# Optimization experiments

Hardware: AMD Instinct MI355X
Metric: run time of the kernel (lower is better)

## Reference

```python
import jax, jax.numpy as jnp
import numpy as np

B, C, H, W = 8192, 3, 32, 32
IN_FEATURES = C * H * W  # 3072, hardcoded in the module


def setup_inputs() -> dict:
    key = jax.random.key(0)
    k1, k2 = jax.random.split(key)
    x = jax.random.normal(k1, (B, C, H, W), dtype=jnp.float32)
    noise = jax.random.normal(k2, (B, C, H, W), dtype=jnp.float32)  # randn_like(x)
    logvar_t = jnp.array([-1.0], dtype=jnp.float32)  # nn.Parameter init
    return {"x": x, "noise": noise, "logvar_t": logvar_t}


def reference(x, noise, logvar_t):
    # additive branch of view_learner.forward
    n_batch = x.shape[0]
    x_t = x + jnp.exp(0.5 * logvar_t[0]) * noise
    var = jnp.exp(logvar_t[0]) + 1e-10
    xf = x.reshape(n_batch, IN_FEATURES)
    # compute_distances: x_norm + x_t_norm - 2 * x @ x.T, clamped to [0, inf)
    x_norm = jnp.sum(xf * xf, axis=1)  # [B]
    dist = x_norm[:, None] + x_norm[None, :] - 2.0 * (xf @ xf.T)  # [B, B]
    dist = jnp.maximum(dist, 0.0)
    distance_contribution = -jnp.mean(jax.nn.logsumexp(-0.5 * dist / var, axis=1))
    normalization_constant = jnp.log(jnp.float32(n_batch))
    kl_xt = (normalization_constant + distance_contribution) / jnp.log(jnp.float32(2.0))
    return x_t, kl_xt
```

## Files before the change

kernel.cpp:

```cpp
#include <hip/hip_runtime.h>
#include <cstdint>

#define K_DIM 3072
#define B_DIM 8192
#define ROW_B 3072
#define ROW_U 768
#define BT    128
#define NTT   64
#define NKT   48

typedef __attribute__((ext_vector_type(4))) float f32x4;
typedef __attribute__((ext_vector_type(4))) int   i32x4;

#define QS     16.0f
#define INV_S2 0.00390625f

__device__ __forceinline__ int q8(float f) {
    int q = __float2int_rn(f * QS);
    return max(-127, min(127, q));
}
__device__ __forceinline__ unsigned pack4(float a, float b, float c, float d) {
    return (unsigned)(q8(a) & 0xFF)
         | ((unsigned)(q8(b) & 0xFF) << 8)
         | ((unsigned)(q8(c) & 0xFF) << 16)
         | ((unsigned)(q8(d) & 0xFF) << 24);
}

__global__ __launch_bounds__(384) void prep_kernel(const float* __restrict__ x,
                                                   const float* __restrict__ nz,
                                                   const float* __restrict__ logvar,
                                                   float* __restrict__ xt,
                                                   unsigned int* __restrict__ xb,
                                                   float* __restrict__ xn,
                                                   float* __restrict__ se)
{
    const int row = blockIdx.x;
    const int tid = threadIdx.x;
    const float4* xr = (const float4*)(x + (size_t)row * K_DIM);
    float4 v0 = xr[2 * tid];
    float4 v1 = xr[2 * tid + 1];
    float s = v0.x * v0.x + v0.y * v0.y + v0.z * v0.z + v0.w * v0.w
            + v1.x * v1.x + v1.y * v1.y + v1.z * v1.z + v1.w * v1.w;

    if (xt) {
        const float4* nr = (const float4*)(nz + (size_t)row * K_DIM);
        float4 n0 = nr[2 * tid], n1 = nr[2 * tid + 1];
        const float sc = __expf(0.5f * logvar[0]);
        float4 o0, o1;
        o0.x = fmaf(sc, n0.x, v0.x); o0.y = fmaf(sc, n0.y, v0.y);
        o0.z = fmaf(sc, n0.z, v0.z); o0.w = fmaf(sc, n0.w, v0.w);
        o1.x = fmaf(sc, n1.x, v1.x); o1.y = fmaf(sc, n1.y, v1.y);
        o1.z = fmaf(sc, n1.z, v1.z); o1.w = fmaf(sc, n1.w, v1.w);
        float4* tr = (float4*)(xt + (size_t)row * K_DIM);
        tr[2 * tid] = o0;
        tr[2 * tid + 1] = o1;
    }

    unsigned int* dst = xb + (size_t)row * ROW_U + tid * 2;
    dst[0] = pack4(v0.x, v0.y, v0.z, v0.w);
    dst[1] = pack4(v1.x, v1.y, v1.z, v1.w);

#pragma unroll
    for (int d = 32; d > 0; d >>= 1) s += __shfl_down(s, d);
    __shared__ float red[6];
    if ((tid & 63) == 0) red[tid >> 6] = s;
    __syncthreads();
    if (tid == 0) {
        float t = 0.f;
#pragma unroll
        for (int i = 0; i < 6; ++i) t += red[i];
        xn[row] = t;
        se[row] = 0.f;
    }
}

struct Frags { i32x4 a[4]; i32x4 b[4]; };

__global__ __launch_bounds__(256, 3) void gram_lse_kernel(const unsigned int* __restrict__ xb,
                                                          const float* __restrict__ xn,
                                                          const float* __restrict__ logvar,
                                                          float* __restrict__ se)
{
    __shared__ __align__(1024) unsigned char lds[3][16384];

    int rem = blockIdx.x;
    int bm = 0;
    while (rem >= NTT - bm) { rem -= NTT - bm; ++bm; }
    const int bn = bm + rem;

    const int tid  = threadIdx.x;
    const int lane = tid & 63;
    const int wave = tid >> 6;
    const int wr = wave >> 1, wc = wave & 1;
    const int fc = lane >> 4;

    const size_t rowA0 = (size_t)bm * BT;
    const size_t rowB0 = (size_t)bn * BT;
    const unsigned char* xb8 = (const unsigned char*)xb;

    unsigned int srcOff[4];
    int dstOff[4];
#pragma unroll
    for (int l = 0; l < 4; ++l) {
        const int e = (l & 1) * 256 + tid;
        const int r = e >> 2, c = e & 3;
        const int csw = c ^ ((r >> 1) & 3);
        const size_t rb = ((l < 2) ? rowA0 : rowB0) + (size_t)r;
        srcOff[l] = (unsigned int)(rb * ROW_B + (size_t)csw * 16);
        dstOff[l] = ((l < 2) ? 0 : 8192) + e * 16;
    }

    i32x4 acc[4][4];
#pragma unroll
    for (int i = 0; i < 4; ++i)
#pragma unroll
        for (int j = 0; j < 4; ++j) acc[i][j] = (i32x4){0, 0, 0, 0};

    int aOff[4], bOff[4];
#pragma unroll
    for (int mi = 0; mi < 4; ++mi) {
        const int r = wr * 64 + mi * 16 + (lane & 15);
        aOff[mi] = r * 64 + (fc ^ ((r >> 1) & 3)) * 16;
    }
#pragma unroll
    for (int ni = 0; ni < 4; ++ni) {
        const int r = wc * 64 + ni * 16 + (lane & 15);
        bOff[ni] = 8192 + r * 64 + (fc ^ ((r >> 1) & 3)) * 16;
    }

#pragma unroll
    for (int l = 0; l < 4; ++l)
        __builtin_amdgcn_global_load_lds(
            (const __attribute__((address_space(1))) void*)(xb8 + srcOff[l]),
            (__attribute__((address_space(3))) void*)(&lds[0][0] + dstOff[l]), 16, 0, 0);
#pragma unroll
    for (int l = 0; l < 4; ++l)
        __builtin_amdgcn_global_load_lds(
            (const __attribute__((address_space(1))) void*)(xb8 + srcOff[l] + 64u),
            (__attribute__((address_space(3))) void*)(&lds[1][0] + dstOff[l]), 16, 0, 0);
    asm volatile("s_waitcnt vmcnt(4)" ::: "memory");
    asm volatile("s_barrier" ::: "memory");

    Frags fA, fB;
#pragma unroll
    for (int mi = 0; mi < 4; ++mi) fA.a[mi] = *(const i32x4*)(&lds[0][0] + aOff[mi]);
#pragma unroll
    for (int ni = 0; ni < 4; ++ni) fA.b[ni] = *(const i32x4*)(&lds[0][0] + bOff[ni]);

    auto body = [&](int t, Frags& cur, Frags& nxt) {
        if (t + 2 < NKT) {
            unsigned char* buf = &lds[(t + 2) % 3][0];
            const unsigned int kg = (unsigned int)(t + 2) * 64u;
#pragma unroll
            for (int l = 0; l < 4; ++l)
                __builtin_amdgcn_global_load_lds(
                    (const __attribute__((address_space(1))) void*)(xb8 + srcOff[l] + kg),
                    (__attribute__((address_space(3))) void*)(buf + dstOff[l]), 16, 0, 0);
        }
        asm volatile("s_waitcnt lgkmcnt(0)" ::: "memory");
        if (t + 2 < NKT)
            asm volatile("s_waitcnt vmcnt(4)" ::: "memory");
        else
            asm volatile("s_waitcnt vmcnt(0)" ::: "memory");
        asm volatile("s_barrier" ::: "memory");
        if (t + 1 < NKT) {
            const unsigned char* buf = &lds[(t + 1) % 3][0];
#pragma unroll
            for (int mi = 0; mi < 4; ++mi) nxt.a[mi] = *(const i32x4*)(buf + aOff[mi]);
#pragma unroll
            for (int ni = 0; ni < 4; ++ni) nxt.b[ni] = *(const i32x4*)(buf + bOff[ni]);
        }
        __builtin_amdgcn_s_setprio(1);
#pragma unroll
        for (int mi = 0; mi < 4; ++mi)
#pragma unroll
            for (int ni = 0; ni < 4; ++ni)
                acc[mi][ni] = __builtin_amdgcn_mfma_i32_16x16x64_i8(
                    cur.a[mi], cur.b[ni], acc[mi][ni], 0, 0, 0);
        __builtin_amdgcn_s_setprio(0);
    };

    for (int tt = 0; tt < NKT / 2; ++tt) {
        body(2 * tt,     fA, fB);
        body(2 * tt + 1, fB, fA);
    }

    const float lv  = logvar[0];
    const float var = __expf(lv) + 1e-10f;
    const float cc  = 0.5f / var;

    const int colBase = (int)rowB0 + wc * 64 + (lane & 15);
    const int rowBase = (int)rowA0 + wr * 64 + (lane >> 4) * 4;

#pragma unroll
    for (int mi = 0; mi < 4; ++mi) {
#pragma unroll
        for (int rg = 0; rg < 4; ++rg) {
            const int i = rowBase + mi * 16 + rg;
            const float xni = xn[i];
            float rs = 0.f;
#pragma unroll
            for (int ni = 0; ni < 4; ++ni) {
                const int j = colBase + ni * 16;
                const float g = (float)acc[mi][ni][rg] * INV_S2;
                const float dist = xni + xn[j] - 2.f * g;
                rs += (i == j) ? 1.0f : __expf(-cc * fmaxf(dist, 0.f));
            }
#pragma unroll
            for (int d = 1; d < 16; d <<= 1) rs += __shfl_xor(rs, d);
            if ((lane & 15) == 0) atomicAdd(&se[i], rs);
        }
    }

    if (bm != bn) {
#pragma unroll
        for (int ni = 0; ni < 4; ++ni) {
            const int j = colBase + ni * 16;
            const float xnj = xn[j];
            float cs = 0.f;
#pragma unroll
            for (int mi = 0; mi < 4; ++mi)
#pragma unroll
                for (int rg = 0; rg < 4; ++rg) {
                    const int i = rowBase + mi * 16 + rg;
                    const float g = (float)acc[mi][ni][rg] * INV_S2;
                    cs += __expf(-cc * fmaxf(xn[i] + xnj - 2.f * g, 0.f));
                }
#pragma unroll
            for (int d = 16; d < 64; d <<= 1) cs += __shfl_xor(cs, d);
            if ((lane >> 4) == 0) atomicAdd(&se[j], cs);
        }
    }
}

__global__ __launch_bounds__(256) void kl_kernel(const float* __restrict__ se,
                                                 float* __restrict__ out)
{
    const int tid = threadIdx.x;
    float s = 0.f;
    for (int i = tid; i < B_DIM; i += 256) s += logf(se[i]);
#pragma unroll
    for (int d = 32; d > 0; d >>= 1) s += __shfl_down(s, d);
    __shared__ float red[4];
    if ((tid & 63) == 0) red[tid >> 6] = s;
    __syncthreads();
    if (tid == 0) {
        const float dc = -(red[0] + red[1] + red[2] + red[3]) / (float)B_DIM;
        out[0] = (logf((float)B_DIM) + dc) / logf(2.f);
    }
}

__global__ __launch_bounds__(256) void xt_kernel(const float4* __restrict__ x,
                                                 const float4* __restrict__ nz,
                                                 const float* __restrict__ logvar,
                                                 float4* __restrict__ out, int n4)
{
    const float sc = expf(0.5f * logvar[0]);
    for (int i = blockIdx.x * blockDim.x + threadIdx.x; i < n4;
         i += gridDim.x * blockDim.x) {
        float4 va = x[i], vb = nz[i];
        float4 o;
        o.x = fmaf(sc, vb.x, va.x);
        o.y = fmaf(sc, vb.y, va.y);
        o.z = fmaf(sc, vb.z, va.z);
        o.w = fmaf(sc, vb.w, va.w);
        out[i] = o;
    }
}

extern "C" void kernel_launch(void* const* d_in, const int* in_sizes, int n_in,
                              void* d_out, int out_size, void* d_ws, size_t ws_size,
                              hipStream_t stream)
{
    const float* x      = (const float*)d_in[0];
    const float* noise  = (const float*)d_in[1];
    const float* logvar = (const float*)d_in[2];
    float* out = (float*)d_out;

    const size_t NEL      = (size_t)B_DIM * K_DIM;
    const size_t XB_BYTES = (size_t)B_DIM * ROW_B;
    const int    NTILES   = NTT * (NTT + 1) / 2;

    const bool use_ws = ws_size >= XB_BYTES + 2 * (size_t)B_DIM * sizeof(float) + 256;

    if (use_ws) {
        unsigned int* xb = (unsigned int*)d_ws;
        float* xn = (float*)((char*)d_ws + XB_BYTES);
        float* se = xn + B_DIM;

        prep_kernel<<<B_DIM, 384, 0, stream>>>(x, noise, logvar, out, xb, xn, se);
        gram_lse_kernel<<<NTILES, 256, 0, stream>>>(xb, xn, logvar, se);
        kl_kernel<<<1, 256, 0, stream>>>(se, out + NEL);
    } else {
        unsigned int* xb = (unsigned int*)d_out;
        float* xn = (float*)((char*)d_out + (32u << 20));
        float* se = xn + B_DIM;

        prep_kernel<<<B_DIM, 384, 0, stream>>>(x, noise, logvar, nullptr, xb, xn, se);
        gram_lse_kernel<<<NTILES, 256, 0, stream>>>(xb, xn, logvar, se);
        kl_kernel<<<1, 256, 0, stream>>>(se, out + NEL);
        xt_kernel<<<2048, 256, 0, stream>>>((const float4*)x, (const float4*)noise,
                                            logvar, (float4*)out, (int)(NEL / 4));
    }
}
```

Measured before the change: 225.9 us.

## Use 256x128 rectangular tiles over the symmetric Gram with XCD-aware block remap

Changes the Gram tile from 128x128 to 256x128, so each wave computes an 8x4 MFMA fragment grid and the A operand is reused across more columns. It also remaps block indices so that consecutive blocks on the same XCD share row strips. The upper-triangle enumeration now works over 128-row half-strips, and waves whose half-strip lies below the diagonal skip the epilogue. The cost is more accumulator registers, larger LDS buffers, and occupancy lowered to 2 blocks per CU, plus some wasted MFMA work on diagonal tiles.

```diff
diff --git a/kernel.cpp b/kernel.cpp
--- a/kernel.cpp
+++ b/kernel.cpp
@@ -5,9 +5,12 @@
 #define B_DIM 8192
 #define ROW_B 3072
 #define ROW_U 768
-#define BT    128
-#define NTT   64
+#define BMA   256
+#define BNB   128
+#define NTB   64
 #define NKT   48
+#define ABYTES 16384
+#define BUFSZ  24576
 
 typedef __attribute__((ext_vector_type(4))) float f32x4;
 typedef __attribute__((ext_vector_type(4))) int   i32x4;
@@ -74,19 +77,20 @@
     }
 }
 
-struct Frags { i32x4 a[4]; i32x4 b[4]; };
-
-__global__ __launch_bounds__(256, 3) void gram_lse_kernel(const unsigned int* __restrict__ xb,
+struct Frags { i32x4 a[8]; i32x4 b[4]; };
+
+__global__ __launch_bounds__(256, 2) void gram_lse_kernel(const unsigned int* __restrict__ xb,
                                                           const float* __restrict__ xn,
                                                           const float* __restrict__ logvar,
                                                           float* __restrict__ se)
 {
-    __shared__ __align__(1024) unsigned char lds[3][16384];
-
-    int rem = blockIdx.x;
-    int bm = 0;
-    while (rem >= NTT - bm) { rem -= NTT - bm; ++bm; }
-    const int bn = bm + rem;
+    __shared__ __align__(1024) unsigned char lds[3][BUFSZ];
+
+    const int orig = blockIdx.x;
+    int rem = (orig & 7) * 132 + (orig >> 3);
+    int a = 0;
+    while (rem >= NTB - 2 * a) { rem -= NTB - 2 * a; ++a; }
+    const int v = 2 * a + rem;
 
     const int tid  = threadIdx.x;
     const int lane = tid & 63;
@@ -94,85 +98,80 @@
     const int wr = wave >> 1, wc = wave & 1;
     const int fc = lane >> 4;
 
-    const size_t rowA0 = (size_t)bm * BT;
-    const size_t rowB0 = (size_t)bn * BT;
+    const size_t rowA0 = (size_t)a * BMA;
+    const size_t rowB0 = (size_t)v * BNB;
     const unsigned char* xb8 = (const unsigned char*)xb;
 
-    unsigned int srcOff[4];
-    int dstOff[4];
-#pragma unroll
-    for (int l = 0; l < 4; ++l) {
-        const int e = (l & 1) * 256 + tid;
+    unsigned int srcOff[6];
+    int dstOff[6];
+#pragma unroll
+    for (int l = 0; l < 6; ++l) {
+        const int e = (l < 4) ? (l * 256 + tid) : ((l - 4) * 256 + tid);
         const int r = e >> 2, c = e & 3;
         const int csw = c ^ ((r >> 1) & 3);
-        const size_t rb = ((l < 2) ? rowA0 : rowB0) + (size_t)r;
+        const size_t rb = ((l < 4) ? rowA0 : rowB0) + (size_t)r;
         srcOff[l] = (unsigned int)(rb * ROW_B + (size_t)csw * 16);
-        dstOff[l] = ((l < 2) ? 0 : 8192) + e * 16;
-    }
-
-    i32x4 acc[4][4];
-#pragma unroll
-    for (int i = 0; i < 4; ++i)
-#pragma unroll
-        for (int j = 0; j < 4; ++j) acc[i][j] = (i32x4){0, 0, 0, 0};
-
-    int aOff[4], bOff[4];
-#pragma unroll
-    for (int mi = 0; mi < 4; ++mi) {
-        const int r = wr * 64 + mi * 16 + (lane & 15);
+        dstOff[l] = ((l < 4) ? 0 : ABYTES) + e * 16;
+    }
+
+    int aOff[8], bOff[4];
+#pragma unroll
+    for (int mi = 0; mi < 8; ++mi) {
+        const int r = wr * 128 + mi * 16 + (lane & 15);
         aOff[mi] = r * 64 + (fc ^ ((r >> 1) & 3)) * 16;
     }
 #pragma unroll
     for (int ni = 0; ni < 4; ++ni) {
         const int r = wc * 64 + ni * 16 + (lane & 15);
-        bOff[ni] = 8192 + r * 64 + (fc ^ ((r >> 1) & 3)) * 16;
-    }
-
-#pragma unroll
-    for (int l = 0; l < 4; ++l)
-        __builtin_amdgcn_global_load_lds(
-            (const __attribute__((address_space(1))) void*)(xb8 + srcOff[l]),
-            (__attribute__((address_space(3))) void*)(&lds[0][0] + dstOff[l]), 16, 0, 0);
-#pragma unroll
-    for (int l = 0; l < 4; ++l)
-        __builtin_amdgcn_global_load_lds(
-            (const __attribute__((address_space(1))) void*)(xb8 + srcOff[l] + 64u),
-            (__attribute__((address_space(3))) void*)(&lds[1][0] + dstOff[l]), 16, 0, 0);
-    asm volatile("s_waitcnt vmcnt(4)" ::: "memory");
+        bOff[ni] = ABYTES + r * 64 + (fc ^ ((r >> 1) & 3)) * 16;
+    }
+
+    i32x4 acc[8][4];
+#pragma unroll
+    for (int i = 0; i < 8; ++i)
+#pragma unroll
+        for (int j = 0; j < 4; ++j) acc[i][j] = (i32x4){0, 0, 0, 0};
+
+#define GLOAD(l, t, buf)                                                          \
+    __builtin_amdgcn_global_load_lds(                                             \
+        (const __attribute__((address_space(1))) void*)(xb8 + srcOff[l] + (unsigned)(t) * 64u), \
+        (__attribute__((address_space(3))) void*)(&lds[buf][0] + dstOff[l]), 16, 0, 0)
+
+#pragma unroll
+    for (int l = 0; l < 6; ++l) GLOAD(l, 0, 0);
+#pragma unroll
+    for (int l = 0; l < 6; ++l) GLOAD(l, 1, 1);
+    asm volatile("s_waitcnt vmcnt(6)" ::: "memory");
     asm volatile("s_barrier" ::: "memory");
 
     Frags fA, fB;
 #pragma unroll
-    for (int mi = 0; mi < 4; ++mi) fA.a[mi] = *(const i32x4*)(&lds[0][0] + aOff[mi]);
+    for (int mi = 0; mi < 8; ++mi) fA.a[mi] = *(const i32x4*)(&lds[0][0] + aOff[mi]);
 #pragma unroll
     for (int ni = 0; ni < 4; ++ni) fA.b[ni] = *(const i32x4*)(&lds[0][0] + bOff[ni]);
 
     auto body = [&](int t, Frags& cur, Frags& nxt) {
         if (t + 2 < NKT) {
-            unsigned char* buf = &lds[(t + 2) % 3][0];
-            const unsigned int kg = (unsigned int)(t + 2) * 64u;
-#pragma unroll
-            for (int l = 0; l < 4; ++l)
-                __builtin_amdgcn_global_load_lds(
-                    (const __attribute__((address_space(1))) void*)(xb8 + srcOff[l] + kg),
-                    (__attribute__((address_space(3))) void*)(buf + dstOff[l]), 16, 0, 0);
+            const int nb = (t + 2) % 3;
+#pragma unroll
+            for (int l = 0; l < 6; ++l) GLOAD(l, t + 2, nb);
         }
         asm volatile("s_waitcnt lgkmcnt(0)" ::: "memory");
         if (t + 2 < NKT)
-            asm volatile("s_waitcnt vmcnt(4)" ::: "memory");
+            asm volatile("s_waitcnt vmcnt(6)" ::: "memory");
         else
             asm volatile("s_waitcnt vmcnt(0)" ::: "memory");
         asm volatile("s_barrier" ::: "memory");
         if (t + 1 < NKT) {
             const unsigned char* buf = &lds[(t + 1) % 3][0];
 #pragma unroll
-            for (int mi = 0; mi < 4; ++mi) nxt.a[mi] = *(const i32x4*)(buf + aOff[mi]);
+            for (int mi = 0; mi < 8; ++mi) nxt.a[mi] = *(const i32x4*)(buf + aOff[mi]);
 #pragma unroll
             for (int ni = 0; ni < 4; ++ni) nxt.b[ni] = *(const i32x4*)(buf + bOff[ni]);
         }
         __builtin_amdgcn_s_setprio(1);
 #pragma unroll
-        for (int mi = 0; mi < 4; ++mi)
+        for (int mi = 0; mi < 8; ++mi)
 #pragma unroll
             for (int ni = 0; ni < 4; ++ni)
                 acc[mi][ni] = __builtin_amdgcn_mfma_i32_16x16x64_i8(
@@ -184,16 +183,20 @@
         body(2 * tt,     fA, fB);
         body(2 * tt + 1, fB, fA);
     }
+#undef GLOAD
 
     const float lv  = logvar[0];
     const float var = __expf(lv) + 1e-10f;
     const float cc  = 0.5f / var;
 
+    const int u = 2 * a + wr;
+    if (u > v) return;
+
     const int colBase = (int)rowB0 + wc * 64 + (lane & 15);
-    const int rowBase = (int)rowA0 + wr * 64 + (lane >> 4) * 4;
-
-#pragma unroll
-    for (int mi = 0; mi < 4; ++mi) {
+    const int rowBase = (int)rowA0 + wr * 128 + (lane >> 4) * 4;
+
+#pragma unroll
+    for (int mi = 0; mi < 8; ++mi) {
 #pragma unroll
         for (int rg = 0; rg < 4; ++rg) {
             const int i = rowBase + mi * 16 + rg;
@@ -212,14 +215,14 @@
         }
     }
 
-    if (bm != bn) {
+    if (u < v) {
 #pragma unroll
         for (int ni = 0; ni < 4; ++ni) {
             const int j = colBase + ni * 16;
             const float xnj = xn[j];
             float cs = 0.f;
 #pragma unroll
-            for (int mi = 0; mi < 4; ++mi)
+            for (int mi = 0; mi < 8; ++mi)
 #pragma unroll
                 for (int rg = 0; rg < 4; ++rg) {
                     const int i = rowBase + mi * 16 + rg;
@@ -279,7 +282,7 @@
 
     const size_t NEL      = (size_t)B_DIM * K_DIM;
     const size_t XB_BYTES = (size_t)B_DIM * ROW_B;
-    const int    NTILES   = NTT * (NTT + 1) / 2;
+    const int    NTILES   = 1056;
 
     const bool use_ws = ws_size >= XB_BYTES + 2 * (size_t)B_DIM * sizeof(float) + 256;
 
```

Measured after the change: 237.0 us. +4.9%, slower.
